# Kernel tuning notes

Hardware: AMD Instinct MI355X
Metric: run time of the kernel (lower is better)

The kernel has to match this reference:

```python
import jax, jax.numpy as jnp
import numpy as np

CAPACITY_FACTOR = 1.25
TOP_K = 2


def setup_inputs() -> dict:
    key = jax.random.key(0)
    ks = jax.random.split(key, 4)
    B, T, D, H, N = 8, 8192, 512, 512, 32
    x = jax.random.normal(ks[0], (B, T, D), jnp.float32)
    Wg = jax.random.normal(ks[1], (D, N), jnp.float32) * 0.02   # gate (no bias)
    W1 = jax.random.normal(ks[2], (N, D, H), jnp.float32) * 0.02  # stacked expert fc1
    b1 = jnp.zeros((N, H), jnp.float32)
    W2 = jax.random.normal(ks[3], (N, H, D), jnp.float32) * 0.02  # stacked expert fc2
    b2 = jnp.zeros((N, D), jnp.float32)
    return {"x": x, "Wg": Wg, "W1": W1, "b1": b1, "W2": W2, "b2": b2}


def _moe(x, Wg, W1, b1, W2, b2):
    B, T, D = x.shape
    N = Wg.shape[1]
    K = TOP_K
    BT = B * T
    BTK = BT * K
    C = int(np.ceil(CAPACITY_FACTOR * BTK / N))  # capacity per expert (static)

    x_flat = x.reshape(BT, D)
    probs = jax.nn.softmax(x_flat @ Wg, axis=-1)            # [BT, N]
    vals, idx = jax.lax.top_k(probs, K)                     # [BT, K]
    vals = vals / jnp.clip(vals.sum(-1, keepdims=True), 1e-9)  # normalize_gates

    # Assignments in the exact order of the original double loop: pos-major, j-minor.
    a = idx.reshape(BTK)                                    # expert id per assignment
    oh = jax.nn.one_hot(a, N, dtype=jnp.int32)              # [BTK, N]
    rank = jnp.cumsum(oh, axis=0) - oh                      # prior count for each expert
    pos = jnp.take_along_axis(rank, a[:, None], axis=1)[:, 0]  # slot within expert
    keep = pos < C                                          # capacity-limited dispatch
    dest = jnp.where(keep, a * C + pos, N * C)              # OOB sentinel -> dropped
    token = jnp.arange(BTK) // K                            # source token per assignment

    # Dispatch: scatter kept tokens into per-expert capacity buffers [N, C, D].
    buf = jnp.zeros((N * C, D), x.dtype).at[dest].set(x_flat[token], mode="drop")
    buf = buf.reshape(N, C, D)

    # Expert FFN (grouped GEMMs). FeedForwardExpert assumed Linear-ReLU-Linear.
    h = jax.nn.relu(jnp.einsum("ncd,ndh->nch", buf, W1) + b1[:, None, :])
    o = (jnp.einsum("nch,nhd->ncd", h, W2) + b2[:, None, :]).reshape(N * C, D)

    # Combine: gather expert outputs, weight by gates, scatter-add back by token.
    gathered = o[jnp.minimum(dest, N * C - 1)]              # dropped rows zeroed via w
    w = vals.reshape(BTK) * keep.astype(x.dtype)
    y_flat = jax.ops.segment_sum(gathered * w[:, None], token, num_segments=BT)
    contrib = jax.ops.segment_sum(w, token, num_segments=BT)
    # Tokens with no surviving assignment pass through unchanged.
    y_flat = jnp.where(contrib[:, None] <= 1e-12, x_flat, y_flat)
    return y_flat.reshape(B, T, D)


def reference(x, Wg, W1, b1, W2, b2):
    return _moe(x, Wg, W1, b1, W2, b2)
```

## Files before the change

### kernel.cpp

```cpp
#include <hip/hip_runtime.h>
#include <hip/hip_bf16.h>

#define BT 65536
#define DD 512
#define HH 512
#define NE 32
#define CAP 5120
#define BM 64
#define NRB 80

typedef float  f32x4  __attribute__((ext_vector_type(4)));
typedef short  bf16x8 __attribute__((ext_vector_type(8)));

__device__ __forceinline__ unsigned short f2bf(float f){
    unsigned int u = __builtin_bit_cast(unsigned int, f);
    unsigned int r = (u + 0x7fffu + ((u >> 16) & 1u)) >> 16;
    return (unsigned short)r;
}

__global__ __launch_bounds__(256) void k_wconv(
    const float* __restrict__ W1, const float* __restrict__ W2,
    unsigned short* __restrict__ W1f, unsigned short* __restrict__ W2f)
{
    int b = blockIdx.x;
    int w = b >> 8;
    int e = (b >> 3) & 31;
    int kq = b & 7;
    const float* src = (w ? W2 : W1) + ((size_t)e << 18);
    unsigned short* dst = (w ? W2f : W1f) + ((size_t)e << 18);
    int t = threadIdx.x;
    #pragma unroll 1
    for (int kg = 0; kg < 8; kg++){
        int k0 = kq*64 + kg*8;
        #pragma unroll
        for (int ng = 0; ng < 2; ng++){
            int n = ng*256 + t;
            unsigned short v[8];
            #pragma unroll
            for (int j = 0; j < 8; j++)
                v[j] = f2bf(src[(size_t)(k0 + j)*512 + n]);
            int nt = n >> 4, kc = k0 >> 5, ln = ((k0 >> 3) & 3)*16 + (n & 15);
            *(bf16x8*)(dst + (((size_t)(nt*16 + kc)*64 + ln) << 3)) = *(bf16x8*)v;
        }
    }
}

__global__ __launch_bounds__(256) void k_gate(
    const float* __restrict__ x, const float* __restrict__ Wg,
    int* __restrict__ counts, int* __restrict__ gsl, float* __restrict__ wts,
    unsigned char* __restrict__ flags)
{
    __shared__ float pacc[4][64][36];
    __shared__ int lcnt[NE], lbase[NE];

    int tid = threadIdx.x;
    int l   = tid & 63;
    int q   = __builtin_amdgcn_readfirstlane(tid >> 6);

    const float* xq = x + ((size_t)(blockIdx.x*64 + l))*DD + q*128;

    float acc[NE];
    #pragma unroll
    for (int n = 0; n < NE; n++) acc[n] = 0.f;

    float4 xa = *(const float4*)(xq);
    float4 xb = *(const float4*)(xq + 4);
    #pragma unroll 1
    for (int d = 0; d < 128; d += 8){
        int dn = (d + 8 < 128) ? (d + 8) : 0;
        float4 na = *(const float4*)(xq + dn);
        float4 nb = *(const float4*)(xq + dn + 4);
        #pragma unroll
        for (int j = 0; j < 8; j++){
            float xv = (j < 4) ? ((j==0)?xa.x:(j==1)?xa.y:(j==2)?xa.z:xa.w)
                               : ((j==4)?xb.x:(j==5)?xb.y:(j==6)?xb.z:xb.w);
            const float4* wr = (const float4*)(Wg + (size_t)(q*128 + d + j)*NE);
            #pragma unroll
            for (int p = 0; p < 8; p++){
                float4 w4 = wr[p];
                acc[p*4+0] = fmaf(xv, w4.x, acc[p*4+0]);
                acc[p*4+1] = fmaf(xv, w4.y, acc[p*4+1]);
                acc[p*4+2] = fmaf(xv, w4.z, acc[p*4+2]);
                acc[p*4+3] = fmaf(xv, w4.w, acc[p*4+3]);
            }
        }
        xa = na; xb = nb;
    }

    #pragma unroll
    for (int n4 = 0; n4 < 8; n4++){
        float4 v; v.x = acc[n4*4]; v.y = acc[n4*4+1]; v.z = acc[n4*4+2]; v.w = acc[n4*4+3];
        *(float4*)&pacc[q][l][n4*4] = v;
    }
    if (tid < NE) lcnt[tid] = 0;
    __syncthreads();

    bool owner = (q == (l & 3));
    int tok = blockIdx.x*64 + l;
    int i1 = 0, i2 = 0, g1 = 0, g2 = 0;
    float w1 = 0.f, w2 = 0.f;

    if (owner){
        #pragma unroll
        for (int n4 = 0; n4 < 8; n4++){
            float4 p0 = *(float4*)&pacc[0][l][n4*4];
            float4 p1 = *(float4*)&pacc[1][l][n4*4];
            float4 p2 = *(float4*)&pacc[2][l][n4*4];
            float4 p3 = *(float4*)&pacc[3][l][n4*4];
            acc[n4*4+0] = (p0.x + p1.x) + (p2.x + p3.x);
            acc[n4*4+1] = (p0.y + p1.y) + (p2.y + p3.y);
            acc[n4*4+2] = (p0.z + p1.z) + (p2.z + p3.z);
            acc[n4*4+3] = (p0.w + p1.w) + (p2.w + p3.w);
        }

        float v1 = -1e30f; i1 = -1;
        #pragma unroll
        for (int n = 0; n < NE; n++) if (acc[n] > v1){ v1 = acc[n]; i1 = n; }
        float v2 = -1e30f; i2 = -1;
        #pragma unroll
        for (int n = 0; n < NE; n++) if (n != i1 && acc[n] > v2){ v2 = acc[n]; i2 = n; }
        float v3 = -1e30f;
        #pragma unroll
        for (int n = 0; n < NE; n++) if (n != i1 && n != i2 && acc[n] > v3) v3 = acc[n];

        if (v2 - v3 >= 1e-4f){
            double ex  = exp((double)v2 - (double)v1);
            double inv = 1.0 / (1.0 + ex);
            w1 = (float)inv; w2 = (float)(ex * inv);
        } else {
            const float* xr = x + (size_t)tok * DD;
            float thresh = v2 - 1e-3f;
            unsigned cmask = 0u;
            #pragma unroll
            for (int n = 0; n < NE; n++) cmask |= (acc[n] >= thresh) ? (1u << n) : 0u;
            double dv1 = -1.0e300, dv2 = -1.0e300; int di1 = -1, di2 = -1;
            #pragma unroll 1
            for (int n = 0; n < NE; n++){
                if (!((cmask >> n) & 1u)) continue;
                double s0 = 0.0, s1 = 0.0, s2 = 0.0, s3 = 0.0;
                #pragma unroll 4
                for (int d = 0; d < DD; d += 4){
                    s0 = fma((double)xr[d+0], (double)Wg[(size_t)(d+0)*NE + n], s0);
                    s1 = fma((double)xr[d+1], (double)Wg[(size_t)(d+1)*NE + n], s1);
                    s2 = fma((double)xr[d+2], (double)Wg[(size_t)(d+2)*NE + n], s2);
                    s3 = fma((double)xr[d+3], (double)Wg[(size_t)(d+3)*NE + n], s3);
                }
                double s = (s0 + s1) + (s2 + s3);
                if (s > dv1){ dv2 = dv1; di2 = di1; dv1 = s; di1 = n; }
                else if (s > dv2){ dv2 = s; di2 = n; }
            }
            i1 = di1; i2 = di2;
            double ex  = exp(dv2 - dv1);
            double inv = 1.0 / (1.0 + ex);
            w1 = (float)inv; w2 = (float)(ex * inv);
        }
        g1 = atomicAdd(&lcnt[i1], 1);
        g2 = atomicAdd(&lcnt[i2], 1);
    }
    __syncthreads();
    if (tid < NE && lcnt[tid] > 0) lbase[tid] = atomicAdd(&counts[tid], lcnt[tid]);
    __syncthreads();
    if (owner){
        g1 += lbase[i1];
        g2 += lbase[i2];
        bool k1 = g1 < CAP, k2 = g2 < CAP;
        if (k1){ gsl[i1*CAP + g1] = tok;               wts[i1*CAP + g1] = w1; }
        if (k2){ gsl[i2*CAP + g2] = tok | (1 << 20);   wts[i2*CAP + g2] = w2; }
        flags[tok] = (unsigned char)((k1 ? 1 : 0) | (k2 ? 2 : 0));
    }
}

__global__ __launch_bounds__(512, 4) void k_ffn(
    const float* __restrict__ x,
    const unsigned short* __restrict__ W1f,
    const unsigned short* __restrict__ W2f,
    const float* __restrict__ b1, const float* __restrict__ b2,
    const int* __restrict__ counts,
    const int* __restrict__ gsl, const float* __restrict__ wts,
    float* __restrict__ y, float* __restrict__ y2)
{
    __shared__ unsigned char AH[64 * 1024];

    int p  = blockIdx.x;
    int s  = p >> 3;
    int e  = ((s / NRB) << 3) | (p & 7);
    int rb = s % NRB;

    int cnt = counts[e]; if (cnt > CAP) cnt = CAP;
    int r0 = rb * BM;
    if (r0 >= cnt) return;

    int tid  = threadIdx.x;
    int lane = tid & 63;
    int wv   = tid >> 6;
    int lg   = lane >> 4;
    int ll   = lane & 15;

    {
        int row = tid >> 3, seg = tid & 7;
        int gr  = r0 + row;
        char* rowb = (char*)AH + row * 1024;
        int rsw = (row & 7) << 4;
        if (gr < cnt){
            int tk = gsl[e*CAP + gr] & 0xFFFFF;
            const float4* src = (const float4*)(x + (size_t)tk*DD + seg*64);
            #pragma unroll
            for (int j = 0; j < 8; j++){
                float4 f0 = src[2*j], f1 = src[2*j+1];
                bf16x8 pk;
                pk[0]=(short)f2bf(f0.x); pk[1]=(short)f2bf(f0.y); pk[2]=(short)f2bf(f0.z); pk[3]=(short)f2bf(f0.w);
                pk[4]=(short)f2bf(f1.x); pk[5]=(short)f2bf(f1.y); pk[6]=(short)f2bf(f1.z); pk[7]=(short)f2bf(f1.w);
                int chunk = seg*8 + j;
                *(bf16x8*)(rowb + ((chunk << 4) ^ rsw)) = pk;
            }
        } else {
            bf16x8 zz = (bf16x8)0;
            #pragma unroll
            for (int j = 0; j < 8; j++){
                int chunk = seg*8 + j;
                *(bf16x8*)(rowb + ((chunk << 4) ^ rsw)) = zz;
            }
        }
    }
    __syncthreads();

    f32x4 acc[4][4];
    #pragma unroll
    for (int a2 = 0; a2 < 4; a2++)
        #pragma unroll
        for (int tt = 0; tt < 4; tt++)
            acc[a2][tt] = (f32x4)0.f;

    {
        const unsigned short* Wa = W1f + ((size_t)e << 18) + (size_t)wv*32768;
        bf16x8 f0[4], f1[4];
        #pragma unroll
        for (int a2 = 0; a2 < 4; a2++)
            f0[a2] = *(const bf16x8*)(Wa + a2*8192 + lane*8);
        #pragma unroll 1
        for (int c = 0; c < 16; c += 2){
            #pragma unroll
            for (int a2 = 0; a2 < 4; a2++)
                f1[a2] = *(const bf16x8*)(Wa + a2*8192 + (c+1)*512 + lane*8);
            {
                bf16x8 bx[4];
                #pragma unroll
                for (int tt = 0; tt < 4; tt++){
                    int tok = tt*16 + ll;
                    int bofs = (64*c + 16*lg) ^ ((tok & 7) << 4);
                    bx[tt] = *(const bf16x8*)((char*)AH + tok*1024 + bofs);
                }
                #pragma unroll
                for (int a2 = 0; a2 < 4; a2++)
                    #pragma unroll
                    for (int tt = 0; tt < 4; tt++)
                        acc[a2][tt] = __builtin_amdgcn_mfma_f32_16x16x32_bf16(f0[a2], bx[tt], acc[a2][tt], 0, 0, 0);
            }
            if (c + 2 < 16){
                #pragma unroll
                for (int a2 = 0; a2 < 4; a2++)
                    f0[a2] = *(const bf16x8*)(Wa + a2*8192 + (c+2)*512 + lane*8);
            }
            {
                bf16x8 bx[4];
                #pragma unroll
                for (int tt = 0; tt < 4; tt++){
                    int tok = tt*16 + ll;
                    int bofs = (64*(c+1) + 16*lg) ^ ((tok & 7) << 4);
                    bx[tt] = *(const bf16x8*)((char*)AH + tok*1024 + bofs);
                }
                #pragma unroll
                for (int a2 = 0; a2 < 4; a2++)
                    #pragma unroll
                    for (int tt = 0; tt < 4; tt++)
                        acc[a2][tt] = __builtin_amdgcn_mfma_f32_16x16x32_bf16(f1[a2], bx[tt], acc[a2][tt], 0, 0, 0);
            }
        }
    }
    __syncthreads();

    #pragma unroll
    for (int a2 = 0; a2 < 4; a2++){
        int n0 = wv*64 + a2*16 + lg*4;
        float4 bv = *(const float4*)(b1 + e*HH + n0);
        #pragma unroll
        for (int tt = 0; tt < 4; tt++){
            int tok = tt*16 + ll;
            float h0 = acc[a2][tt][0] + bv.x; h0 = h0 > 0.f ? h0 : 0.f;
            float h1 = acc[a2][tt][1] + bv.y; h1 = h1 > 0.f ? h1 : 0.f;
            float h2 = acc[a2][tt][2] + bv.z; h2 = h2 > 0.f ? h2 : 0.f;
            float h3 = acc[a2][tt][3] + bv.w; h3 = h3 > 0.f ? h3 : 0.f;
            uint2 pk;
            pk.x = (unsigned)f2bf(h0) | ((unsigned)f2bf(h1) << 16);
            pk.y = (unsigned)f2bf(h2) | ((unsigned)f2bf(h3) << 16);
            int bofs = (n0*2) ^ ((tok & 7) << 4);
            *(uint2*)((char*)AH + tok*1024 + bofs) = pk;
            acc[a2][tt] = (f32x4)0.f;
        }
    }
    __syncthreads();

    {
        const unsigned short* Wb = W2f + ((size_t)e << 18) + (size_t)wv*32768;
        bf16x8 f0[4], f1[4];
        #pragma unroll
        for (int b_ = 0; b_ < 4; b_++)
            f0[b_] = *(const bf16x8*)(Wb + b_*8192 + lane*8);
        #pragma unroll 1
        for (int kc = 0; kc < 16; kc += 2){
            #pragma unroll
            for (int b_ = 0; b_ < 4; b_++)
                f1[b_] = *(const bf16x8*)(Wb + b_*8192 + (kc+1)*512 + lane*8);
            {
                bf16x8 ah[4];
                #pragma unroll
                for (int tt = 0; tt < 4; tt++){
                    int tok = tt*16 + ll;
                    int bofs = (64*kc + 16*lg) ^ ((tok & 7) << 4);
                    ah[tt] = *(const bf16x8*)((char*)AH + tok*1024 + bofs);
                }
                #pragma unroll
                for (int b_ = 0; b_ < 4; b_++)
                    #pragma unroll
                    for (int tt = 0; tt < 4; tt++)
                        acc[b_][tt] = __builtin_amdgcn_mfma_f32_16x16x32_bf16(ah[tt], f0[b_], acc[b_][tt], 0, 0, 0);
            }
            if (kc + 2 < 16){
                #pragma unroll
                for (int b_ = 0; b_ < 4; b_++)
                    f0[b_] = *(const bf16x8*)(Wb + b_*8192 + (kc+2)*512 + lane*8);
            }
            {
                bf16x8 ah[4];
                #pragma unroll
                for (int tt = 0; tt < 4; tt++){
                    int tok = tt*16 + ll;
                    int bofs = (64*(kc+1) + 16*lg) ^ ((tok & 7) << 4);
                    ah[tt] = *(const bf16x8*)((char*)AH + tok*1024 + bofs);
                }
                #pragma unroll
                for (int b_ = 0; b_ < 4; b_++)
                    #pragma unroll
                    for (int tt = 0; tt < 4; tt++)
                        acc[b_][tt] = __builtin_amdgcn_mfma_f32_16x16x32_bf16(ah[tt], f1[b_], acc[b_][tt], 0, 0, 0);
            }
        }
    }

    float bb[4];
    #pragma unroll
    for (int b_ = 0; b_ < 4; b_++)
        bb[b_] = b2[e*DD + wv*64 + b_*16 + ll];

    #pragma unroll
    for (int tt = 0; tt < 4; tt++){
        #pragma unroll
        for (int i = 0; i < 4; i++){
            int rl = tt*16 + lg*4 + i;
            int gr = r0 + rl;
            if (gr < cnt){
                int   v  = gsl[e*CAP + gr];
                int   tk = v & 0xFFFFF;
                float w  = wts[e*CAP + gr];
                float* dst = ((v >> 20) ? y2 : y) + (size_t)tk * DD;
                #pragma unroll
                for (int b_ = 0; b_ < 4; b_++){
                    int col = wv*64 + b_*16 + ll;
                    dst[col] = w * (acc[b_][tt][i] + bb[b_]);
                }
            }
        }
    }
}

__global__ __launch_bounds__(256) void k_comb(
    const float* __restrict__ x, const float* __restrict__ y2,
    const unsigned char* __restrict__ flags, float* __restrict__ y)
{
    const float4* x4  = (const float4*)x;
    const float4* y24 = (const float4*)y2;
    float4* y4 = (float4*)y;
    int nthreads = gridDim.x * 256;
    int g = blockIdx.x * 256 + threadIdx.x;
    #pragma unroll 1
    for (long long idx = g; idx < (long long)BT * 128; idx += nthreads){
        int t = (int)(idx >> 7);
        int f = flags[t];
        if (f == 3){
            float4 a = y4[idx], b = y24[idx];
            a.x += b.x; a.y += b.y; a.z += b.z; a.w += b.w;
            y4[idx] = a;
        } else if (f == 2){
            y4[idx] = y24[idx];
        } else if (f == 0){
            y4[idx] = x4[idx];
        }
    }
}

extern "C" void kernel_launch(void* const* d_in, const int* in_sizes, int n_in,
                              void* d_out, int out_size, void* d_ws, size_t ws_size,
                              hipStream_t stream)
{
    const float* x  = (const float*)d_in[0];
    const float* Wg = (const float*)d_in[1];
    const float* W1 = (const float*)d_in[2];
    const float* b1 = (const float*)d_in[3];
    const float* W2 = (const float*)d_in[4];
    const float* b2 = (const float*)d_in[5];
    float* y = (float*)d_out;

    char* ws = (char*)d_ws;
    unsigned short* W1f = (unsigned short*)(ws);
    unsigned short* W2f = (unsigned short*)(ws + 16777216);
    int*   counts = (int*)  (ws + 33554432);
    int*   gsl    = (int*)  (ws + 33554432 + 256);
    float* wts    = (float*)(ws + 33554432 + 256 + 655360);
    unsigned char* flags = (unsigned char*)(ws + 33554432 + 256 + 2*655360);
    float* y2     = (float*)(ws + 35651584);

    hipMemsetAsync(counts, 0, 256, stream);
    hipLaunchKernelGGL(k_wconv, dim3(512), dim3(256), 0, stream, W1, W2, W1f, W2f);
    hipLaunchKernelGGL(k_gate,  dim3(BT/64), dim3(256), 0, stream, x, Wg, counts, gsl, wts, flags);
    hipLaunchKernelGGL(k_ffn,   dim3(NE*NRB), dim3(512), 0, stream, x, W1f, W2f, b1, b2, counts, gsl, wts, y, y2);
    hipLaunchKernelGGL(k_comb,  dim3(2048), dim3(256), 0, stream, x, y2, flags, y);
}
```

Measured before the change: 417.3 us.

## Double FFN row tile to 128, overlap x staging, store second output in bf16

Each k_ffn block now handles 128 tokens instead of 64, so every expert weight fragment loaded from global memory feeds twice as many MFMAs. The second half of the x rows is converted and staged into LDS while the first GEMM's early k-chunks run, which changes the LDS layout to two 512-byte-per-row halves for stage one. The second-choice expert output y2 is written as bf16 and widened in k_comb, halving that intermediate's traffic at some precision cost. The larger accumulator set and 128 KB of LDS force occupancy down to two blocks per CU.

```diff
diff --git a/kernel.cpp b/kernel.cpp
--- a/kernel.cpp
+++ b/kernel.cpp
@@ -6,8 +6,8 @@
 #define HH 512
 #define NE 32
 #define CAP 5120
-#define BM 64
-#define NRB 80
+#define BM 128
+#define NRB 40
 
 typedef float  f32x4  __attribute__((ext_vector_type(4)));
 typedef short  bf16x8 __attribute__((ext_vector_type(8)));
@@ -16,6 +16,10 @@
     unsigned int u = __builtin_bit_cast(unsigned int, f);
     unsigned int r = (u + 0x7fffu + ((u >> 16) & 1u)) >> 16;
     return (unsigned short)r;
+}
+__device__ __forceinline__ float bf2f(unsigned short h){
+    unsigned int u = ((unsigned int)h) << 16;
+    return __builtin_bit_cast(float, u);
 }
 
 __global__ __launch_bounds__(256) void k_wconv(
@@ -170,16 +174,16 @@
     }
 }
 
-__global__ __launch_bounds__(512, 4) void k_ffn(
+__global__ __launch_bounds__(512, 2) void k_ffn(
     const float* __restrict__ x,
     const unsigned short* __restrict__ W1f,
     const unsigned short* __restrict__ W2f,
     const float* __restrict__ b1, const float* __restrict__ b2,
     const int* __restrict__ counts,
     const int* __restrict__ gsl, const float* __restrict__ wts,
-    float* __restrict__ y, float* __restrict__ y2)
+    float* __restrict__ y, unsigned short* __restrict__ y2h)
 {
-    __shared__ unsigned char AH[64 * 1024];
+    __shared__ unsigned char AH[131072];
 
     int p  = blockIdx.x;
     int s  = p >> 3;
@@ -196,39 +200,37 @@
     int lg   = lane >> 4;
     int ll   = lane & 15;
 
-    {
-        int row = tid >> 3, seg = tid & 7;
-        int gr  = r0 + row;
-        char* rowb = (char*)AH + row * 1024;
-        int rsw = (row & 7) << 4;
-        if (gr < cnt){
-            int tk = gsl[e*CAP + gr] & 0xFFFFF;
-            const float4* src = (const float4*)(x + (size_t)tk*DD + seg*64);
-            #pragma unroll
-            for (int j = 0; j < 8; j++){
-                float4 f0 = src[2*j], f1 = src[2*j+1];
-                bf16x8 pk;
-                pk[0]=(short)f2bf(f0.x); pk[1]=(short)f2bf(f0.y); pk[2]=(short)f2bf(f0.z); pk[3]=(short)f2bf(f0.w);
-                pk[4]=(short)f2bf(f1.x); pk[5]=(short)f2bf(f1.y); pk[6]=(short)f2bf(f1.z); pk[7]=(short)f2bf(f1.w);
-                int chunk = seg*8 + j;
-                *(bf16x8*)(rowb + ((chunk << 4) ^ rsw)) = pk;
-            }
-        } else {
-            bf16x8 zz = (bf16x8)0;
-            #pragma unroll
-            for (int j = 0; j < 8; j++){
-                int chunk = seg*8 + j;
-                *(bf16x8*)(rowb + ((chunk << 4) ^ rsw)) = zz;
-            }
-        }
-    }
-    __syncthreads();
-
-    f32x4 acc[4][4];
+    int srow = tid >> 2, sseg = tid & 3;
+    int sgr  = r0 + srow;
+    bool svalid = sgr < cnt;
+    int stk = svalid ? (gsl[e*CAP + sgr] & 0xFFFFF) : 0;
+    const float* sx = x + (size_t)stk*DD + sseg*64;
+    char* srowb = (char*)AH + srow*512;
+    int ssw = (srow & 7) << 4;
+
+    #pragma unroll 4
+    for (int i = 0; i < 8; i++){
+        float4 v0, v1;
+        if (svalid){ v0 = *(const float4*)(sx + i*8); v1 = *(const float4*)(sx + i*8 + 4); }
+        else { v0.x=v0.y=v0.z=v0.w=0.f; v1=v0; }
+        uint2 pk;
+        pk.x = (unsigned)f2bf(v0.x) | ((unsigned)f2bf(v0.y) << 16);
+        pk.y = (unsigned)f2bf(v0.z) | ((unsigned)f2bf(v0.w) << 16);
+        uint2 pk2;
+        pk2.x = (unsigned)f2bf(v1.x) | ((unsigned)f2bf(v1.y) << 16);
+        pk2.y = (unsigned)f2bf(v1.z) | ((unsigned)f2bf(v1.w) << 16);
+        int dl = sseg*64 + i*8;
+        int cl = dl >> 3;
+        *(uint2*)(srowb + ((cl ^ (srow & 7)) << 4))     = pk;
+        *(uint2*)(srowb + ((cl ^ (srow & 7)) << 4) + 8) = pk2;
+    }
+    __syncthreads();
+
+    f32x4 acc[4][8];
     #pragma unroll
     for (int a2 = 0; a2 < 4; a2++)
         #pragma unroll
-        for (int tt = 0; tt < 4; tt++)
+        for (int tt = 0; tt < 8; tt++)
             acc[a2][tt] = (f32x4)0.f;
 
     {
@@ -242,39 +244,51 @@
             #pragma unroll
             for (int a2 = 0; a2 < 4; a2++)
                 f1[a2] = *(const bf16x8*)(Wa + a2*8192 + (c+1)*512 + lane*8);
-            {
-                bf16x8 bx[4];
-                #pragma unroll
-                for (int tt = 0; tt < 4; tt++){
-                    int tok = tt*16 + ll;
-                    int bofs = (64*c + 16*lg) ^ ((tok & 7) << 4);
-                    bx[tt] = *(const bf16x8*)((char*)AH + tok*1024 + bofs);
-                }
-                #pragma unroll
-                for (int a2 = 0; a2 < 4; a2++)
-                    #pragma unroll
-                    for (int tt = 0; tt < 4; tt++)
-                        acc[a2][tt] = __builtin_amdgcn_mfma_f32_16x16x32_bf16(f0[a2], bx[tt], acc[a2][tt], 0, 0, 0);
+            if (c < 8){
+                #pragma unroll
+                for (int u = 0; u < 4; u++){
+                    int i = (c >> 1)*4 + u;
+                    float4 v;
+                    if (svalid) v = *(const float4*)(sx + 256 + i*4);
+                    else { v.x=v.y=v.z=v.w=0.f; }
+                    uint2 pk;
+                    pk.x = (unsigned)f2bf(v.x) | ((unsigned)f2bf(v.y) << 16);
+                    pk.y = (unsigned)f2bf(v.z) | ((unsigned)f2bf(v.w) << 16);
+                    int dl = sseg*64 + i*4;
+                    int cl = dl >> 3;
+                    *(uint2*)(srowb + 65536 + ((cl ^ (srow & 7)) << 4) + (dl & 7)*2) = pk;
+                }
+            }
+            #pragma unroll
+            for (int tp = 0; tp < 4; tp++){
+                int cc = c*4 + lg, hf = cc >> 5, cl = cc & 31;
+                int t0 = tp*32 + ll, t1 = tp*32 + 16 + ll;
+                bf16x8 bx0 = *(const bf16x8*)((char*)AH + hf*65536 + t0*512 + ((cl ^ (t0 & 7)) << 4));
+                bf16x8 bx1 = *(const bf16x8*)((char*)AH + hf*65536 + t1*512 + ((cl ^ (t1 & 7)) << 4));
+                #pragma unroll
+                for (int a2 = 0; a2 < 4; a2++){
+                    acc[a2][tp*2]   = __builtin_amdgcn_mfma_f32_16x16x32_bf16(f0[a2], bx0, acc[a2][tp*2],   0, 0, 0);
+                    acc[a2][tp*2+1] = __builtin_amdgcn_mfma_f32_16x16x32_bf16(f0[a2], bx1, acc[a2][tp*2+1], 0, 0, 0);
+                }
             }
             if (c + 2 < 16){
                 #pragma unroll
                 for (int a2 = 0; a2 < 4; a2++)
                     f0[a2] = *(const bf16x8*)(Wa + a2*8192 + (c+2)*512 + lane*8);
             }
-            {
-                bf16x8 bx[4];
-                #pragma unroll
-                for (int tt = 0; tt < 4; tt++){
-                    int tok = tt*16 + ll;
-                    int bofs = (64*(c+1) + 16*lg) ^ ((tok & 7) << 4);
-                    bx[tt] = *(const bf16x8*)((char*)AH + tok*1024 + bofs);
-                }
-                #pragma unroll
-                for (int a2 = 0; a2 < 4; a2++)
-                    #pragma unroll
-                    for (int tt = 0; tt < 4; tt++)
-                        acc[a2][tt] = __builtin_amdgcn_mfma_f32_16x16x32_bf16(f1[a2], bx[tt], acc[a2][tt], 0, 0, 0);
-            }
+            #pragma unroll
+            for (int tp = 0; tp < 4; tp++){
+                int cc = (c+1)*4 + lg, hf = cc >> 5, cl = cc & 31;
+                int t0 = tp*32 + ll, t1 = tp*32 + 16 + ll;
+                bf16x8 bx0 = *(const bf16x8*)((char*)AH + hf*65536 + t0*512 + ((cl ^ (t0 & 7)) << 4));
+                bf16x8 bx1 = *(const bf16x8*)((char*)AH + hf*65536 + t1*512 + ((cl ^ (t1 & 7)) << 4));
+                #pragma unroll
+                for (int a2 = 0; a2 < 4; a2++){
+                    acc[a2][tp*2]   = __builtin_amdgcn_mfma_f32_16x16x32_bf16(f1[a2], bx0, acc[a2][tp*2],   0, 0, 0);
+                    acc[a2][tp*2+1] = __builtin_amdgcn_mfma_f32_16x16x32_bf16(f1[a2], bx1, acc[a2][tp*2+1], 0, 0, 0);
+                }
+            }
+            if (c == 6) __syncthreads();
         }
     }
     __syncthreads();
@@ -284,7 +298,7 @@
         int n0 = wv*64 + a2*16 + lg*4;
         float4 bv = *(const float4*)(b1 + e*HH + n0);
         #pragma unroll
-        for (int tt = 0; tt < 4; tt++){
+        for (int tt = 0; tt < 8; tt++){
             int tok = tt*16 + ll;
             float h0 = acc[a2][tt][0] + bv.x; h0 = h0 > 0.f ? h0 : 0.f;
             float h1 = acc[a2][tt][1] + bv.y; h1 = h1 > 0.f ? h1 : 0.f;
@@ -311,38 +325,34 @@
             #pragma unroll
             for (int b_ = 0; b_ < 4; b_++)
                 f1[b_] = *(const bf16x8*)(Wb + b_*8192 + (kc+1)*512 + lane*8);
-            {
-                bf16x8 ah[4];
-                #pragma unroll
-                for (int tt = 0; tt < 4; tt++){
-                    int tok = tt*16 + ll;
-                    int bofs = (64*kc + 16*lg) ^ ((tok & 7) << 4);
-                    ah[tt] = *(const bf16x8*)((char*)AH + tok*1024 + bofs);
-                }
-                #pragma unroll
-                for (int b_ = 0; b_ < 4; b_++)
-                    #pragma unroll
-                    for (int tt = 0; tt < 4; tt++)
-                        acc[b_][tt] = __builtin_amdgcn_mfma_f32_16x16x32_bf16(ah[tt], f0[b_], acc[b_][tt], 0, 0, 0);
+            #pragma unroll
+            for (int tp = 0; tp < 4; tp++){
+                int bo = (kc*4 + lg) << 4;
+                int t0 = tp*32 + ll, t1 = tp*32 + 16 + ll;
+                bf16x8 a0 = *(const bf16x8*)((char*)AH + t0*1024 + (bo ^ ((t0 & 7) << 4)));
+                bf16x8 a1 = *(const bf16x8*)((char*)AH + t1*1024 + (bo ^ ((t1 & 7) << 4)));
+                #pragma unroll
+                for (int b_ = 0; b_ < 4; b_++){
+                    acc[b_][tp*2]   = __builtin_amdgcn_mfma_f32_16x16x32_bf16(a0, f0[b_], acc[b_][tp*2],   0, 0, 0);
+                    acc[b_][tp*2+1] = __builtin_amdgcn_mfma_f32_16x16x32_bf16(a1, f0[b_], acc[b_][tp*2+1], 0, 0, 0);
+                }
             }
             if (kc + 2 < 16){
                 #pragma unroll
                 for (int b_ = 0; b_ < 4; b_++)
                     f0[b_] = *(const bf16x8*)(Wb + b_*8192 + (kc+2)*512 + lane*8);
             }
-            {
-                bf16x8 ah[4];
-                #pragma unroll
-                for (int tt = 0; tt < 4; tt++){
-                    int tok = tt*16 + ll;
-                    int bofs = (64*(kc+1) + 16*lg) ^ ((tok & 7) << 4);
-                    ah[tt] = *(const bf16x8*)((char*)AH + tok*1024 + bofs);
-                }
-                #pragma unroll
-                for (int b_ = 0; b_ < 4; b_++)
-                    #pragma unroll
-                    for (int tt = 0; tt < 4; tt++)
-                        acc[b_][tt] = __builtin_amdgcn_mfma_f32_16x16x32_bf16(ah[tt], f1[b_], acc[b_][tt], 0, 0, 0);
+            #pragma unroll
+            for (int tp = 0; tp < 4; tp++){
+                int bo = ((kc+1)*4 + lg) << 4;
+                int t0 = tp*32 + ll, t1 = tp*32 + 16 + ll;
+                bf16x8 a0 = *(const bf16x8*)((char*)AH + t0*1024 + (bo ^ ((t0 & 7) << 4)));
+                bf16x8 a1 = *(const bf16x8*)((char*)AH + t1*1024 + (bo ^ ((t1 & 7) << 4)));
+                #pragma unroll
+                for (int b_ = 0; b_ < 4; b_++){
+                    acc[b_][tp*2]   = __builtin_amdgcn_mfma_f32_16x16x32_bf16(a0, f1[b_], acc[b_][tp*2],   0, 0, 0);
+                    acc[b_][tp*2+1] = __builtin_amdgcn_mfma_f32_16x16x32_bf16(a1, f1[b_], acc[b_][tp*2+1], 0, 0, 0);
+                }
             }
         }
     }
@@ -353,7 +363,7 @@
         bb[b_] = b2[e*DD + wv*64 + b_*16 + ll];
 
     #pragma unroll
-    for (int tt = 0; tt < 4; tt++){
+    for (int tt = 0; tt < 8; tt++){
         #pragma unroll
         for (int i = 0; i < 4; i++){
             int rl = tt*16 + lg*4 + i;
@@ -362,11 +372,20 @@
                 int   v  = gsl[e*CAP + gr];
                 int   tk = v & 0xFFFFF;
                 float w  = wts[e*CAP + gr];
-                float* dst = ((v >> 20) ? y2 : y) + (size_t)tk * DD;
-                #pragma unroll
-                for (int b_ = 0; b_ < 4; b_++){
-                    int col = wv*64 + b_*16 + ll;
-                    dst[col] = w * (acc[b_][tt][i] + bb[b_]);
+                if (v >> 20){
+                    unsigned short* dst = y2h + (size_t)tk * DD;
+                    #pragma unroll
+                    for (int b_ = 0; b_ < 4; b_++){
+                        int col = wv*64 + b_*16 + ll;
+                        dst[col] = f2bf(w * (acc[b_][tt][i] + bb[b_]));
+                    }
+                } else {
+                    float* dst = y + (size_t)tk * DD;
+                    #pragma unroll
+                    for (int b_ = 0; b_ < 4; b_++){
+                        int col = wv*64 + b_*16 + ll;
+                        dst[col] = w * (acc[b_][tt][i] + bb[b_]);
+                    }
                 }
             }
         }
@@ -374,11 +393,11 @@
 }
 
 __global__ __launch_bounds__(256) void k_comb(
-    const float* __restrict__ x, const float* __restrict__ y2,
+    const float* __restrict__ x, const unsigned short* __restrict__ y2h,
     const unsigned char* __restrict__ flags, float* __restrict__ y)
 {
     const float4* x4  = (const float4*)x;
-    const float4* y24 = (const float4*)y2;
+    const uint2*  y24 = (const uint2*)y2h;
     float4* y4 = (float4*)y;
     int nthreads = gridDim.x * 256;
     int g = blockIdx.x * 256 + threadIdx.x;
@@ -387,11 +406,21 @@
         int t = (int)(idx >> 7);
         int f = flags[t];
         if (f == 3){
-            float4 a = y4[idx], b = y24[idx];
-            a.x += b.x; a.y += b.y; a.z += b.z; a.w += b.w;
+            float4 a = y4[idx];
+            uint2 p = y24[idx];
+            a.x += bf2f((unsigned short)(p.x & 0xFFFF));
+            a.y += bf2f((unsigned short)(p.x >> 16));
+            a.z += bf2f((unsigned short)(p.y & 0xFFFF));
+            a.w += bf2f((unsigned short)(p.y >> 16));
             y4[idx] = a;
         } else if (f == 2){
-            y4[idx] = y24[idx];
+            uint2 p = y24[idx];
+            float4 a;
+            a.x = bf2f((unsigned short)(p.x & 0xFFFF));
+            a.y = bf2f((unsigned short)(p.x >> 16));
+            a.z = bf2f((unsigned short)(p.y & 0xFFFF));
+            a.w = bf2f((unsigned short)(p.y >> 16));
+            y4[idx] = a;
         } else if (f == 0){
             y4[idx] = x4[idx];
         }
@@ -417,11 +446,11 @@
     int*   gsl    = (int*)  (ws + 33554432 + 256);
     float* wts    = (float*)(ws + 33554432 + 256 + 655360);
     unsigned char* flags = (unsigned char*)(ws + 33554432 + 256 + 2*655360);
-    float* y2     = (float*)(ws + 35651584);
+    unsigned short* y2h  = (unsigned short*)(ws + 35651584);
 
     hipMemsetAsync(counts, 0, 256, stream);
     hipLaunchKernelGGL(k_wconv, dim3(512), dim3(256), 0, stream, W1, W2, W1f, W2f);
     hipLaunchKernelGGL(k_gate,  dim3(BT/64), dim3(256), 0, stream, x, Wg, counts, gsl, wts, flags);
-    hipLaunchKernelGGL(k_ffn,   dim3(NE*NRB), dim3(512), 0, stream, x, W1f, W2f, b1, b2, counts, gsl, wts, y, y2);
-    hipLaunchKernelGGL(k_comb,  dim3(2048), dim3(256), 0, stream, x, y2, flags, y);
-}
+    hipLaunchKernelGGL(k_ffn,   dim3(NE*NRB), dim3(512), 0, stream, x, W1f, W2f, b1, b2, counts, gsl, wts, y, y2h);
+    hipLaunchKernelGGL(k_comb,  dim3(2048), dim3(256), 0, stream, x, y2h, flags, y);
+}
```

Measured after the change: 443.9 us. +6.4%, slower.

## Fuse weight conversion into gate kernel, precast x to bf16, store second output in bf16

Applied to the files above, without the earlier changes.

Merges the weight-conversion and gating kernels into one launch. The gate pass now also writes a bf16 copy of x, so the FFN gather reads half the bytes and skips per-row conversion. The second-slot expert outputs are stored as bf16 and widened in the combine kernel, which halves that intermediate's traffic. In exchange the gate pass does an extra 64MB write, and the second-slot contribution loses precision from bf16 rounding.

```diff
diff --git a/kernel.cpp b/kernel.cpp
--- a/kernel.cpp
+++ b/kernel.cpp
@@ -17,47 +17,53 @@
     unsigned int r = (u + 0x7fffu + ((u >> 16) & 1u)) >> 16;
     return (unsigned short)r;
 }
-
-__global__ __launch_bounds__(256) void k_wconv(
+__device__ __forceinline__ float bf2f(unsigned short h){
+    unsigned int u = ((unsigned int)h) << 16;
+    return __builtin_bit_cast(float, u);
+}
+
+__global__ __launch_bounds__(256) void k_prep(
+    const float* __restrict__ x, const float* __restrict__ Wg,
     const float* __restrict__ W1, const float* __restrict__ W2,
-    unsigned short* __restrict__ W1f, unsigned short* __restrict__ W2f)
-{
-    int b = blockIdx.x;
-    int w = b >> 8;
-    int e = (b >> 3) & 31;
-    int kq = b & 7;
-    const float* src = (w ? W2 : W1) + ((size_t)e << 18);
-    unsigned short* dst = (w ? W2f : W1f) + ((size_t)e << 18);
-    int t = threadIdx.x;
-    #pragma unroll 1
-    for (int kg = 0; kg < 8; kg++){
-        int k0 = kq*64 + kg*8;
-        #pragma unroll
-        for (int ng = 0; ng < 2; ng++){
-            int n = ng*256 + t;
-            unsigned short v[8];
-            #pragma unroll
-            for (int j = 0; j < 8; j++)
-                v[j] = f2bf(src[(size_t)(k0 + j)*512 + n]);
-            int nt = n >> 4, kc = k0 >> 5, ln = ((k0 >> 3) & 3)*16 + (n & 15);
-            *(bf16x8*)(dst + (((size_t)(nt*16 + kc)*64 + ln) << 3)) = *(bf16x8*)v;
-        }
-    }
-}
-
-__global__ __launch_bounds__(256) void k_gate(
-    const float* __restrict__ x, const float* __restrict__ Wg,
+    unsigned short* __restrict__ W1f, unsigned short* __restrict__ W2f,
     int* __restrict__ counts, int* __restrict__ gsl, float* __restrict__ wts,
-    unsigned char* __restrict__ flags)
+    unsigned char* __restrict__ flags, unsigned short* __restrict__ xb16)
 {
     __shared__ float pacc[4][64][36];
     __shared__ int lcnt[NE], lbase[NE];
 
     int tid = threadIdx.x;
+
+    if (blockIdx.x < 512){
+        int b = blockIdx.x;
+        int w = b >> 8;
+        int e = (b >> 3) & 31;
+        int kq = b & 7;
+        const float* src = (w ? W2 : W1) + ((size_t)e << 18);
+        unsigned short* dst = (w ? W2f : W1f) + ((size_t)e << 18);
+        #pragma unroll 1
+        for (int kg = 0; kg < 8; kg++){
+            int k0 = kq*64 + kg*8;
+            #pragma unroll
+            for (int ng = 0; ng < 2; ng++){
+                int n = ng*256 + tid;
+                unsigned short v[8];
+                #pragma unroll
+                for (int j = 0; j < 8; j++)
+                    v[j] = f2bf(src[(size_t)(k0 + j)*512 + n]);
+                int nt = n >> 4, kc = k0 >> 5, ln = ((k0 >> 3) & 3)*16 + (n & 15);
+                *(bf16x8*)(dst + (((size_t)(nt*16 + kc)*64 + ln) << 3)) = *(bf16x8*)v;
+            }
+        }
+        return;
+    }
+
+    int blk = blockIdx.x - 512;
     int l   = tid & 63;
     int q   = __builtin_amdgcn_readfirstlane(tid >> 6);
-
-    const float* xq = x + ((size_t)(blockIdx.x*64 + l))*DD + q*128;
+    int tok = blk*64 + l;
+
+    const float* xq = x + (size_t)tok*DD + q*128;
 
     float acc[NE];
     #pragma unroll
@@ -70,6 +76,12 @@
         int dn = (d + 8 < 128) ? (d + 8) : 0;
         float4 na = *(const float4*)(xq + dn);
         float4 nb = *(const float4*)(xq + dn + 4);
+        uint4 pk;
+        pk.x = (unsigned)f2bf(xa.x) | ((unsigned)f2bf(xa.y) << 16);
+        pk.y = (unsigned)f2bf(xa.z) | ((unsigned)f2bf(xa.w) << 16);
+        pk.z = (unsigned)f2bf(xb.x) | ((unsigned)f2bf(xb.y) << 16);
+        pk.w = (unsigned)f2bf(xb.z) | ((unsigned)f2bf(xb.w) << 16);
+        *(uint4*)(xb16 + (size_t)tok*DD + q*128 + d) = pk;
         #pragma unroll
         for (int j = 0; j < 8; j++){
             float xv = (j < 4) ? ((j==0)?xa.x:(j==1)?xa.y:(j==2)?xa.z:xa.w)
@@ -96,7 +108,6 @@
     __syncthreads();
 
     bool owner = (q == (l & 3));
-    int tok = blockIdx.x*64 + l;
     int i1 = 0, i2 = 0, g1 = 0, g2 = 0;
     float w1 = 0.f, w2 = 0.f;
 
@@ -171,13 +182,13 @@
 }
 
 __global__ __launch_bounds__(512, 4) void k_ffn(
-    const float* __restrict__ x,
+    const unsigned short* __restrict__ xb16,
     const unsigned short* __restrict__ W1f,
     const unsigned short* __restrict__ W2f,
     const float* __restrict__ b1, const float* __restrict__ b2,
     const int* __restrict__ counts,
     const int* __restrict__ gsl, const float* __restrict__ wts,
-    float* __restrict__ y, float* __restrict__ y2)
+    float* __restrict__ y, unsigned short* __restrict__ y2h)
 {
     __shared__ unsigned char AH[64 * 1024];
 
@@ -203,22 +214,19 @@
         int rsw = (row & 7) << 4;
         if (gr < cnt){
             int tk = gsl[e*CAP + gr] & 0xFFFFF;
-            const float4* src = (const float4*)(x + (size_t)tk*DD + seg*64);
+            const uint4* src = (const uint4*)(xb16 + (size_t)tk*DD + seg*64);
             #pragma unroll
             for (int j = 0; j < 8; j++){
-                float4 f0 = src[2*j], f1 = src[2*j+1];
-                bf16x8 pk;
-                pk[0]=(short)f2bf(f0.x); pk[1]=(short)f2bf(f0.y); pk[2]=(short)f2bf(f0.z); pk[3]=(short)f2bf(f0.w);
-                pk[4]=(short)f2bf(f1.x); pk[5]=(short)f2bf(f1.y); pk[6]=(short)f2bf(f1.z); pk[7]=(short)f2bf(f1.w);
+                uint4 v = src[j];
                 int chunk = seg*8 + j;
-                *(bf16x8*)(rowb + ((chunk << 4) ^ rsw)) = pk;
+                *(uint4*)(rowb + ((chunk << 4) ^ rsw)) = v;
             }
         } else {
-            bf16x8 zz = (bf16x8)0;
+            uint4 zz; zz.x = zz.y = zz.z = zz.w = 0u;
             #pragma unroll
             for (int j = 0; j < 8; j++){
                 int chunk = seg*8 + j;
-                *(bf16x8*)(rowb + ((chunk << 4) ^ rsw)) = zz;
+                *(uint4*)(rowb + ((chunk << 4) ^ rsw)) = zz;
             }
         }
     }
@@ -362,11 +370,20 @@
                 int   v  = gsl[e*CAP + gr];
                 int   tk = v & 0xFFFFF;
                 float w  = wts[e*CAP + gr];
-                float* dst = ((v >> 20) ? y2 : y) + (size_t)tk * DD;
-                #pragma unroll
-                for (int b_ = 0; b_ < 4; b_++){
-                    int col = wv*64 + b_*16 + ll;
-                    dst[col] = w * (acc[b_][tt][i] + bb[b_]);
+                if (v >> 20){
+                    unsigned short* dst = y2h + (size_t)tk * DD;
+                    #pragma unroll
+                    for (int b_ = 0; b_ < 4; b_++){
+                        int col = wv*64 + b_*16 + ll;
+                        dst[col] = f2bf(w * (acc[b_][tt][i] + bb[b_]));
+                    }
+                } else {
+                    float* dst = y + (size_t)tk * DD;
+                    #pragma unroll
+                    for (int b_ = 0; b_ < 4; b_++){
+                        int col = wv*64 + b_*16 + ll;
+                        dst[col] = w * (acc[b_][tt][i] + bb[b_]);
+                    }
                 }
             }
         }
@@ -374,11 +391,11 @@
 }
 
 __global__ __launch_bounds__(256) void k_comb(
-    const float* __restrict__ x, const float* __restrict__ y2,
+    const float* __restrict__ x, const unsigned short* __restrict__ y2h,
     const unsigned char* __restrict__ flags, float* __restrict__ y)
 {
     const float4* x4  = (const float4*)x;
-    const float4* y24 = (const float4*)y2;
+    const uint2*  y24 = (const uint2*)y2h;
     float4* y4 = (float4*)y;
     int nthreads = gridDim.x * 256;
     int g = blockIdx.x * 256 + threadIdx.x;
@@ -387,11 +404,21 @@
         int t = (int)(idx >> 7);
         int f = flags[t];
         if (f == 3){
-            float4 a = y4[idx], b = y24[idx];
-            a.x += b.x; a.y += b.y; a.z += b.z; a.w += b.w;
+            float4 a = y4[idx];
+            uint2 p = y24[idx];
+            a.x += bf2f((unsigned short)(p.x & 0xFFFF));
+            a.y += bf2f((unsigned short)(p.x >> 16));
+            a.z += bf2f((unsigned short)(p.y & 0xFFFF));
+            a.w += bf2f((unsigned short)(p.y >> 16));
             y4[idx] = a;
         } else if (f == 2){
-            y4[idx] = y24[idx];
+            uint2 p = y24[idx];
+            float4 a;
+            a.x = bf2f((unsigned short)(p.x & 0xFFFF));
+            a.y = bf2f((unsigned short)(p.x >> 16));
+            a.z = bf2f((unsigned short)(p.y & 0xFFFF));
+            a.w = bf2f((unsigned short)(p.y >> 16));
+            y4[idx] = a;
         } else if (f == 0){
             y4[idx] = x4[idx];
         }
@@ -417,11 +444,13 @@
     int*   gsl    = (int*)  (ws + 33554432 + 256);
     float* wts    = (float*)(ws + 33554432 + 256 + 655360);
     unsigned char* flags = (unsigned char*)(ws + 33554432 + 256 + 2*655360);
-    float* y2     = (float*)(ws + 35651584);
+    unsigned short* xb16 = (unsigned short*)(ws + 35651584);
+    unsigned short* y2h  = (unsigned short*)(ws + 35651584 + 67108864);
 
     hipMemsetAsync(counts, 0, 256, stream);
-    hipLaunchKernelGGL(k_wconv, dim3(512), dim3(256), 0, stream, W1, W2, W1f, W2f);
-    hipLaunchKernelGGL(k_gate,  dim3(BT/64), dim3(256), 0, stream, x, Wg, counts, gsl, wts, flags);
-    hipLaunchKernelGGL(k_ffn,   dim3(NE*NRB), dim3(512), 0, stream, x, W1f, W2f, b1, b2, counts, gsl, wts, y, y2);
-    hipLaunchKernelGGL(k_comb,  dim3(2048), dim3(256), 0, stream, x, y2, flags, y);
-}
+    hipLaunchKernelGGL(k_prep, dim3(512 + BT/64), dim3(256), 0, stream,
+                       x, Wg, W1, W2, W1f, W2f, counts, gsl, wts, flags, xb16);
+    hipLaunchKernelGGL(k_ffn,  dim3(NE*NRB), dim3(512), 0, stream,
+                       xb16, W1f, W2f, b1, b2, counts, gsl, wts, y, y2h);
+    hipLaunchKernelGGL(k_comb, dim3(2048), dim3(256), 0, stream, x, y2h, flags, y);
+}
```

Result: no change. 421.6 us (+1.0%).
